# Optimization experiments

Hardware: AMD Instinct MI355X
Metric: run time of the kernel (lower is better)

The kernel has to match this reference:

```python
import jax, jax.numpy as jnp
import numpy as np

N, D, E, K = 8192, 4096, 64, 2

def setup_inputs() -> dict:
    key = jax.random.key(0)
    k1, k2 = jax.random.split(key)
    x = jax.random.normal(k1, (N, D), dtype=jnp.float32)
    W = jax.random.normal(k2, (E, D), dtype=jnp.float32) * (1.0 / np.sqrt(D))
    b = jnp.zeros((E,), dtype=jnp.float32)
    return {"x": x, "W": W, "b": b, "k": K}

def reference(x, W, b, k):
    # logits = x @ W^T + b : [N, E]
    logits = jnp.einsum('nd,ed->ne', x, W) + b
    probs = jax.nn.softmax(logits, axis=1)
    top_w, top_idx = jax.lax.top_k(probs, k)  # [N, k] each
    return (top_idx, top_w)
```

## Files before the change

### kernel.cpp

```cpp
#include <hip/hip_runtime.h>
#include <hip/hip_bf16.h>

#define N_ROWS 8192
#define D_DIM  4096
#define E_DIM  64
#define BR     32
#define BK     256
#define NCH    (D_DIM / BK)
#define NSTEP  (BK / 32)

typedef __attribute__((ext_vector_type(8))) short  short8;
typedef __attribute__((ext_vector_type(4))) float  floatx4;
typedef __attribute__((ext_vector_type(8))) float  float8;

__device__ inline void cvt_split(const float8& f, short8& hi, short8& lo) {
#pragma unroll
  for (int j = 0; j < 8; ++j) {
    float x = f[j];
    unsigned int u  = __builtin_bit_cast(unsigned int, x);
    unsigned int rh = (u + 0x7FFFu + ((u >> 16) & 1u)) >> 16;
    hi[j] = (short)rh;
    float hf = __builtin_bit_cast(float, rh << 16);
    float lf = x - hf;
    unsigned int ul = __builtin_bit_cast(unsigned int, lf);
    lo[j] = (short)(ul >> 16);
  }
}

__global__ __launch_bounds__(512) void prep_w(const void* __restrict__ xv,
                                              const void* __restrict__ wv,
                                              void* __restrict__ ws) {
  __shared__ int sflag;
  const int tid = threadIdx.x;
  if (tid < 64) {
    unsigned int v = ((const unsigned int*)xv)[(size_t)tid * 997];
    unsigned int e = (v >> 7) & 0xFFu;
    unsigned long long m = __ballot(e >= 100u && e <= 140u);
    if (tid == 0) sflag = (__popcll(m) > 32) ? 1 : 0;
  }
  __syncthreads();
  if (sflag) return;
  const int t    = blockIdx.x * 512 + tid;
  const int lane = t & 63;
  const int idx  = t >> 6;
  const int s    = idx >> 2;
  const int e    = idx & 3;
  const int row  = e * 16 + (lane & 15);
  const int col  = s * 32 + (lane >> 4) * 8;
  float8 f = *(const float8*)((const float*)wv + (size_t)row * D_DIM + col);
  short8 h, l;
  cvt_split(f, h, l);
  char* d = (char*)ws + (size_t)idx * 2048 + lane * 16;
  *(short8*)d          = h;
  *(short8*)(d + 1024) = l;
}

__global__ __launch_bounds__(256, 1) void router_kernel(
    const void* __restrict__ xv, const void* __restrict__ wv,
    const void* __restrict__ bv, const void* __restrict__ wsv,
    float* __restrict__ out) {
  __shared__ __align__(16) char sm[2][32768];
  __shared__ float lg[BR][E_DIM + 4];
  __shared__ int   sflag;

  const int tid = threadIdx.x;

  if (tid < 64) {
    unsigned int v = ((const unsigned int*)xv)[(size_t)tid * 997];
    unsigned int e = (v >> 7) & 0xFFu;
    unsigned long long m = __ballot(e >= 100u && e <= 140u);
    if (tid == 0) sflag = (__popcll(m) > 32) ? 1 : 0;
  }
  __syncthreads();
  const int isbf = sflag;

  const int wave = tid >> 6;
  const int lane = tid & 63;
  const int lm   = lane & 15;
  const int t4   = lane >> 4;
  const int r0   = blockIdx.x * BR;

  floatx4 acc0 = {0.f, 0.f, 0.f, 0.f};
  floatx4 acc1 = {0.f, 0.f, 0.f, 0.f};

  if (!isbf) {
    const int srow = tid >> 3;
    const int grp  = tid & 7;
    const float* xg = (const float*)xv + (size_t)(r0 + srow) * D_DIM + grp * 32;
    const int ws0 = srow * 512 + (((grp * 4 + 0) ^ (srow & 7)) << 4);
    const int ws1 = srow * 512 + (((grp * 4 + 1) ^ (srow & 7)) << 4);
    const int ws2 = srow * 512 + (((grp * 4 + 2) ^ (srow & 7)) << 4);
    const int ws3 = srow * 512 + (((grp * 4 + 3) ^ (srow & 7)) << 4);
    const char* wb = (const char*)wsv + (size_t)wave * 2048 + lane * 16;
    const int ra  = lm * 512;
    const int axr = lm & 7;

    short8 bh0, bh1, bh2, bh3, bh4, bh5, bh6, bh7;
    short8 bl0, bl1, bl2, bl3, bl4, bl5, bl6, bl7;

#define LDB(K, BASE)                                                       \
    bh##K = *(const short8*)((BASE) + (size_t)(K) * 8192);                 \
    bl##K = *(const short8*)((BASE) + (size_t)(K) * 8192 + 1024);

#define STAGE(DST, F0, F1, F2, F3)                                         \
    {                                                                      \
      short8 h, l;                                                         \
      cvt_split(F0, h, l); *(short8*)((DST) + ws0) = h;                    \
                           *(short8*)((DST) + 16384 + ws0) = l;            \
      cvt_split(F1, h, l); *(short8*)((DST) + ws1) = h;                    \
                           *(short8*)((DST) + 16384 + ws1) = l;            \
      cvt_split(F2, h, l); *(short8*)((DST) + ws2) = h;                    \
                           *(short8*)((DST) + 16384 + ws2) = l;            \
      cvt_split(F3, h, l); *(short8*)((DST) + ws3) = h;                    \
                           *(short8*)((DST) + 16384 + ws3) = l;            \
    }

    LDB(0, wb) LDB(1, wb) LDB(2, wb) LDB(3, wb)
    LDB(4, wb) LDB(5, wb) LDB(6, wb) LDB(7, wb)
    {
      float8 f0 = *(const float8*)xg;
      float8 f1 = *(const float8*)(xg + 8);
      float8 f2 = *(const float8*)(xg + 16);
      float8 f3 = *(const float8*)(xg + 24);
      STAGE(sm[0], f0, f1, f2, f3)
    }
    asm volatile("s_waitcnt lgkmcnt(0)\n\ts_barrier" ::: "memory");

    for (int i = 0; i < NCH; ++i) {
      float8 f0, f1, f2, f3;
      if (i + 1 < NCH) {
        const int o = (i + 1) * BK;
        f0 = *(const float8*)(xg + o);
        f1 = *(const float8*)(xg + o + 8);
        f2 = *(const float8*)(xg + o + 16);
        f3 = *(const float8*)(xg + o + 24);
      }
      const char* s   = sm[i & 1];
      const char* wbn = wb + (size_t)((i + 1 < NCH) ? i + 1 : i) * (NSTEP * 8192);

#define STEP(K)                                                            \
    {                                                                      \
      const int sa = ((((K) << 2) + t4) ^ axr) << 4;                       \
      short8 ah0 = *(const short8*)(s + ra + sa);                          \
      short8 al0 = *(const short8*)(s + 16384 + ra + sa);                  \
      short8 ah1 = *(const short8*)(s + 8192 + ra + sa);                   \
      short8 al1 = *(const short8*)(s + 24576 + ra + sa);                  \
      acc0 = __builtin_amdgcn_mfma_f32_16x16x32_bf16(ah0, bh##K, acc0, 0, 0, 0); \
      acc0 = __builtin_amdgcn_mfma_f32_16x16x32_bf16(ah0, bl##K, acc0, 0, 0, 0); \
      acc0 = __builtin_amdgcn_mfma_f32_16x16x32_bf16(al0, bh##K, acc0, 0, 0, 0); \
      acc1 = __builtin_amdgcn_mfma_f32_16x16x32_bf16(ah1, bh##K, acc1, 0, 0, 0); \
      acc1 = __builtin_amdgcn_mfma_f32_16x16x32_bf16(ah1, bl##K, acc1, 0, 0, 0); \
      acc1 = __builtin_amdgcn_mfma_f32_16x16x32_bf16(al1, bh##K, acc1, 0, 0, 0); \
      LDB(K, wbn)                                                          \
    }

      STEP(0) STEP(1) STEP(2) STEP(3)
      STEP(4) STEP(5) STEP(6) STEP(7)

      if (i + 1 < NCH) {
        STAGE(sm[(i + 1) & 1], f0, f1, f2, f3)
      }
      asm volatile("s_waitcnt lgkmcnt(0)\n\ts_barrier" ::: "memory");
    }
#undef STEP
#undef STAGE
#undef LDB
  } else {
    const short* xp0 = (const short*)xv + (size_t)(r0 + lm) * D_DIM + t4 * 8;
    const short* xp1 = xp0 + (size_t)16 * D_DIM;
    const short* wp  = (const short*)wv + (size_t)(wave * 16 + lm) * D_DIM + t4 * 8;
    for (int k = 0; k < D_DIM; k += 32) {
      short8 a0 = *(const short8*)(xp0 + k);
      short8 a1 = *(const short8*)(xp1 + k);
      short8 b0 = *(const short8*)(wp + k);
      acc0 = __builtin_amdgcn_mfma_f32_16x16x32_bf16(a0, b0, acc0, 0, 0, 0);
      acc1 = __builtin_amdgcn_mfma_f32_16x16x32_bf16(a1, b0, acc1, 0, 0, 0);
    }
  }

  {
    const int col   = wave * 16 + lm;
    const int rbase = t4 << 2;
#pragma unroll
    for (int r = 0; r < 4; ++r) {
      lg[rbase + r][col]      = acc0[r];
      lg[16 + rbase + r][col] = acc1[r];
    }
  }
  __syncthreads();

  if (tid < BR) {
    const int row = tid;
    float m1 = -3.4e38f, m2 = -3.4e38f;
    int   i1 = 0, i2 = 0;
    for (int e = 0; e < E_DIM; ++e) {
      float be = isbf ? __bfloat162float(((const __hip_bfloat16*)bv)[e])
                      : ((const float*)bv)[e];
      float l = lg[row][e] + be;
      if (l > m1)      { m2 = m1; i2 = i1; m1 = l; i1 = e; }
      else if (l > m2) { m2 = l;  i2 = e; }
    }
    float s = 0.f;
    for (int e = 0; e < E_DIM; ++e) {
      float be = isbf ? __bfloat162float(((const __hip_bfloat16*)bv)[e])
                      : ((const float*)bv)[e];
      s += expf(lg[row][e] + be - m1);
    }
    const int gr = r0 + row;
    out[2 * gr]                  = (float)i1;
    out[2 * gr + 1]              = (float)i2;
    out[2 * N_ROWS + 2 * gr]     = 1.0f / s;
    out[2 * N_ROWS + 2 * gr + 1] = expf(m2 - m1) / s;
  }
}

extern "C" void kernel_launch(void* const* d_in, const int* in_sizes, int n_in,
                              void* d_out, int out_size, void* d_ws, size_t ws_size,
                              hipStream_t stream) {
  (void)in_sizes; (void)n_in; (void)out_size; (void)ws_size;
  prep_w<<<dim3(64), dim3(512), 0, stream>>>(d_in[0], d_in[1], d_ws);
  router_kernel<<<dim3(N_ROWS / BR), dim3(256), 0, stream>>>(
      d_in[0], d_in[1], d_in[2], d_ws, (float*)d_out);
}
```

Baseline: 220.9 us.

## Split the reduction dimension across two wave groups per block

Each block now runs 512 threads as two halves, and each half computes partial logits over one half of the D dimension using its own double-buffered shared tiles. The two partial results are summed in shared memory before the softmax/top-k step. The aim is more waves per CU, which gives more latency hiding and more parallel work on each row tile. The cost is doubled LDS use per block (about 136KB), which may limit occupancy to one block per CU despite the launch bounds asking for two.

Measured after the change: 223.6 us. No clear change (+1.2%).

```diff
diff --git a/kernel.cpp b/kernel.cpp
--- a/kernel.cpp
+++ b/kernel.cpp
@@ -5,8 +5,9 @@
 #define D_DIM  4096
 #define E_DIM  64
 #define BR     32
+#define HALFK  2048
 #define BK     256
-#define NCH    (D_DIM / BK)
+#define NCH    (HALFK / BK)
 #define NSTEP  (BK / 32)
 
 typedef __attribute__((ext_vector_type(8))) short  short8;
@@ -55,12 +56,12 @@
   *(short8*)(d + 1024) = l;
 }
 
-__global__ __launch_bounds__(256, 1) void router_kernel(
+__global__ __launch_bounds__(512, 2) void router_kernel(
     const void* __restrict__ xv, const void* __restrict__ wv,
     const void* __restrict__ bv, const void* __restrict__ wsv,
     float* __restrict__ out) {
-  __shared__ __align__(16) char sm[2][32768];
-  __shared__ float lg[BR][E_DIM + 4];
+  __shared__ __align__(16) char sm[2][2][32768];
+  __shared__ float lg[2][BR][E_DIM + 4];
   __shared__ int   sflag;
 
   const int tid = threadIdx.x;
@@ -75,6 +76,8 @@
   const int isbf = sflag;
 
   const int wave = tid >> 6;
+  const int h    = wave >> 2;
+  const int et   = wave & 3;
   const int lane = tid & 63;
   const int lm   = lane & 15;
   const int t4   = lane >> 4;
@@ -84,14 +87,17 @@
   floatx4 acc1 = {0.f, 0.f, 0.f, 0.f};
 
   if (!isbf) {
-    const int srow = tid >> 3;
-    const int grp  = tid & 7;
-    const float* xg = (const float*)xv + (size_t)(r0 + srow) * D_DIM + grp * 32;
+    const int stid = tid & 255;
+    const int srow = stid >> 3;
+    const int grp  = stid & 7;
+    const float* xg = (const float*)xv +
+        (size_t)(r0 + srow) * D_DIM + h * HALFK + grp * 32;
     const int ws0 = srow * 512 + (((grp * 4 + 0) ^ (srow & 7)) << 4);
     const int ws1 = srow * 512 + (((grp * 4 + 1) ^ (srow & 7)) << 4);
     const int ws2 = srow * 512 + (((grp * 4 + 2) ^ (srow & 7)) << 4);
     const int ws3 = srow * 512 + (((grp * 4 + 3) ^ (srow & 7)) << 4);
-    const char* wb = (const char*)wsv + (size_t)wave * 2048 + lane * 16;
+    const char* wb = (const char*)wsv + (size_t)h * 524288 +
+                     (size_t)et * 2048 + lane * 16;
     const int ra  = lm * 512;
     const int axr = lm & 7;
 
@@ -104,15 +110,15 @@
 
 #define STAGE(DST, F0, F1, F2, F3)                                         \
     {                                                                      \
-      short8 h, l;                                                         \
-      cvt_split(F0, h, l); *(short8*)((DST) + ws0) = h;                    \
-                           *(short8*)((DST) + 16384 + ws0) = l;            \
-      cvt_split(F1, h, l); *(short8*)((DST) + ws1) = h;                    \
-                           *(short8*)((DST) + 16384 + ws1) = l;            \
-      cvt_split(F2, h, l); *(short8*)((DST) + ws2) = h;                    \
-                           *(short8*)((DST) + 16384 + ws2) = l;            \
-      cvt_split(F3, h, l); *(short8*)((DST) + ws3) = h;                    \
-                           *(short8*)((DST) + 16384 + ws3) = l;            \
+      short8 hh, ll;                                                       \
+      cvt_split(F0, hh, ll); *(short8*)((DST) + ws0) = hh;                 \
+                             *(short8*)((DST) + 16384 + ws0) = ll;         \
+      cvt_split(F1, hh, ll); *(short8*)((DST) + ws1) = hh;                 \
+                             *(short8*)((DST) + 16384 + ws1) = ll;         \
+      cvt_split(F2, hh, ll); *(short8*)((DST) + ws2) = hh;                 \
+                             *(short8*)((DST) + 16384 + ws2) = ll;         \
+      cvt_split(F3, hh, ll); *(short8*)((DST) + ws3) = hh;                 \
+                             *(short8*)((DST) + 16384 + ws3) = ll;         \
     }
 
     LDB(0, wb) LDB(1, wb) LDB(2, wb) LDB(3, wb)
@@ -122,7 +128,7 @@
       float8 f1 = *(const float8*)(xg + 8);
       float8 f2 = *(const float8*)(xg + 16);
       float8 f3 = *(const float8*)(xg + 24);
-      STAGE(sm[0], f0, f1, f2, f3)
+      STAGE(sm[h][0], f0, f1, f2, f3)
     }
     asm volatile("s_waitcnt lgkmcnt(0)\n\ts_barrier" ::: "memory");
 
@@ -135,7 +141,7 @@
         f2 = *(const float8*)(xg + o + 16);
         f3 = *(const float8*)(xg + o + 24);
       }
-      const char* s   = sm[i & 1];
+      const char* s   = sm[h][i & 1];
       const char* wbn = wb + (size_t)((i + 1 < NCH) ? i + 1 : i) * (NSTEP * 8192);
 
 #define STEP(K)                                                            \
@@ -158,7 +164,7 @@
       STEP(4) STEP(5) STEP(6) STEP(7)
 
       if (i + 1 < NCH) {
-        STAGE(sm[(i + 1) & 1], f0, f1, f2, f3)
+        STAGE(sm[h][(i + 1) & 1], f0, f1, f2, f3)
       }
       asm volatile("s_waitcnt lgkmcnt(0)\n\ts_barrier" ::: "memory");
     }
@@ -166,10 +172,12 @@
 #undef STAGE
 #undef LDB
   } else {
-    const short* xp0 = (const short*)xv + (size_t)(r0 + lm) * D_DIM + t4 * 8;
+    const short* xp0 = (const short*)xv + (size_t)(r0 + lm) * D_DIM +
+                       h * HALFK + t4 * 8;
     const short* xp1 = xp0 + (size_t)16 * D_DIM;
-    const short* wp  = (const short*)wv + (size_t)(wave * 16 + lm) * D_DIM + t4 * 8;
-    for (int k = 0; k < D_DIM; k += 32) {
+    const short* wp  = (const short*)wv + (size_t)(et * 16 + lm) * D_DIM +
+                       h * HALFK + t4 * 8;
+    for (int k = 0; k < HALFK; k += 32) {
       short8 a0 = *(const short8*)(xp0 + k);
       short8 a1 = *(const short8*)(xp1 + k);
       short8 b0 = *(const short8*)(wp + k);
@@ -179,12 +187,12 @@
   }
 
   {
-    const int col   = wave * 16 + lm;
+    const int col   = et * 16 + lm;
     const int rbase = t4 << 2;
 #pragma unroll
     for (int r = 0; r < 4; ++r) {
-      lg[rbase + r][col]      = acc0[r];
-      lg[16 + rbase + r][col] = acc1[r];
+      lg[h][rbase + r][col]      = acc0[r];
+      lg[h][16 + rbase + r][col] = acc1[r];
     }
   }
   __syncthreads();
@@ -196,7 +204,7 @@
     for (int e = 0; e < E_DIM; ++e) {
       float be = isbf ? __bfloat162float(((const __hip_bfloat16*)bv)[e])
                       : ((const float*)bv)[e];
-      float l = lg[row][e] + be;
+      float l = lg[0][row][e] + lg[1][row][e] + be;
       if (l > m1)      { m2 = m1; i2 = i1; m1 = l; i1 = e; }
       else if (l > m2) { m2 = l;  i2 = e; }
     }
@@ -204,7 +212,7 @@
     for (int e = 0; e < E_DIM; ++e) {
       float be = isbf ? __bfloat162float(((const __hip_bfloat16*)bv)[e])
                       : ((const float*)bv)[e];
-      s += expf(lg[row][e] + be - m1);
+      s += expf(lg[0][row][e] + lg[1][row][e] + be - m1);
     }
     const int gr = r0 + row;
     out[2 * gr]                  = (float)i1;
@@ -219,6 +227,6 @@
                               hipStream_t stream) {
   (void)in_sizes; (void)n_in; (void)out_size; (void)ws_size;
   prep_w<<<dim3(64), dim3(512), 0, stream>>>(d_in[0], d_in[1], d_ws);
-  router_kernel<<<dim3(N_ROWS / BR), dim3(256), 0, stream>>>(
+  router_kernel<<<dim3(N_ROWS / BR), dim3(512), 0, stream>>>(
       d_in[0], d_in[1], d_in[2], d_ws, (float*)d_out);
 }
```
